# Kernel optimization log

Measured on AMD Instinct MI355X. Metric: run time of the kernel, lower is better.

Reference implementation:

```python
import jax, jax.numpy as jnp
import numpy as np

B = 2048
NUM_ITER = 3  # dynamic routing iterations


def _conv2d(x, w, b, pad):
    # x: [B,C,H,W], w: [O,I,kh,kw] (OIHW)
    y = jax.lax.conv_general_dilated(
        x, w, window_strides=(1, 1), padding=[(pad, pad), (pad, pad)],
        dimension_numbers=('NCHW', 'OIHW', 'NCHW'))
    return y + b[None, :, None, None]


def _maxpool2(x):
    return jax.lax.reduce_window(x, -jnp.inf, jax.lax.max,
                                 (1, 1, 2, 2), (1, 1, 2, 2), 'VALID')


def _squash(t, axis=-1):
    # scale = |t|^2/(1+|t|^2); out = scale * t / |t|
    n2 = jnp.sum(t * t, axis=axis, keepdims=True)
    return (n2 / (1.0 + n2)) * t * jax.lax.rsqrt(n2)


def setup_inputs() -> dict:
    key = jax.random.key(0)
    ks = jax.random.split(key, 8)
    f32 = jnp.float32
    rn = lambda k, s, sc=1.0: jax.random.normal(k, s, f32) * sc
    return {
        'x': rn(ks[0], (B, 1, 36, 60)),
        'y': rn(ks[1], (B, 2)),
        'conv1_w': rn(ks[2], (20, 1, 5, 5), 0.1),
        'conv1_b': jnp.zeros((20,), f32),
        'conv2_w': rn(ks[3], (50, 20, 5, 5), 0.01),
        'conv2_b': jnp.zeros((50,), f32),
        'pcaps_w': rn(ks[4], (16, 50, 5, 5), 0.05),   # 4 capsules x 4 out-ch, stacked
        'pcaps_b': jnp.zeros((16,), f32),
        'route_w': rn(ks[5], (2, 288, 4, 1)),          # [num_caps, route_nodes, in_ch, out_ch]
        'fc1_w': rn(ks[6], (500, 3602), 0.02),
        'fc1_b': jnp.zeros((500,), f32),
        'fc2_w': rn(ks[7], (2, 502), 0.05),
        'fc2_b': jnp.zeros((2,), f32),
    }


def reference(x, y, conv1_w, conv1_b, conv2_w, conv2_b, pcaps_w, pcaps_b,
              route_w, fc1_w, fc1_b, fc2_w, fc2_b):
    b = x.shape[0]
    # conv backbone
    h = _maxpool2(_conv2d(x, conv1_w, conv1_b, 0))   # [B,20,16,28]
    h = _maxpool2(_conv2d(h, conv2_w, conv2_b, 0))   # [B,50,6,12]

    # primary capsules: 4 parallel convs (stacked into one), each [B,4,6,12]
    p = _conv2d(h, pcaps_w, pcaps_b, 2)              # [B,16,6,12]
    u = p.reshape(b, 4, 4 * 6 * 12)                  # [B, caps=4, nodes=288] (c,h,w flatten per capsule)
    u = u.transpose(0, 2, 1)                         # [B,288,4]
    u = _squash(u, axis=-1)

    # digit capsules: dynamic routing
    # priors[k,b,r,o] = sum_c u[b,r,c] * W[k,r,c,o]
    priors = jnp.einsum('brc,krco->kbro', u, route_w)  # [2,B,288,1]
    logits = jnp.zeros_like(priors)
    v = None
    for i in range(NUM_ITER):
        probs = jax.nn.softmax(logits, axis=2)
        v = _squash(jnp.sum(probs * priors, axis=2, keepdims=True), axis=-1)  # [2,B,1,1]
        if i < NUM_ITER - 1:
            logits = logits + jnp.sum(priors * v, axis=-1, keepdims=True)

    c = v[:, :, 0, :].transpose(1, 0, 2).reshape(b, -1)  # [B,2]
    xf = h.reshape(b, -1)                                # [B,3600]
    f = jnp.concatenate([xf, c], axis=-1)                # [B,3602]
    f = jax.nn.relu(f @ fc1_w.T + fc1_b)                 # [B,500]
    f = jnp.concatenate([f, y], axis=1)                  # [B,502]
    return f @ fc2_w.T + fc2_b                           # [B,2]
```

## Files before the change

kernel.cpp:

```cpp
#include <hip/hip_runtime.h>
#include <math.h>


#define BATCH 2048
#define KP 3712
#define NPREP 551

typedef __attribute__((ext_vector_type(8))) short short8;
typedef __attribute__((ext_vector_type(4))) float floatx4;
typedef unsigned short u16;
typedef unsigned int   u32;

#define GLD(gp, lp) __builtin_amdgcn_global_load_lds( \
    (const __attribute__((address_space(1))) u32*)(gp), \
    (__attribute__((address_space(3))) u32*)(lp), 16, 0, 0)

__device__ inline float wave_sum(float v) {
#pragma unroll
    for (int off = 32; off >= 1; off >>= 1) v += __shfl_xor(v, off);
    return v;
}
__device__ inline float wave_max(float v) {
#pragma unroll
    for (int off = 32; off >= 1; off >>= 1) v = fmaxf(v, __shfl_xor(v, off));
    return v;
}
__device__ inline u16 f2bf(float f) {
    u32 u = __float_as_uint(f);
    u32 r = (u + 0x7FFFu + ((u >> 16) & 1u)) >> 16;
    return (u16)r;
}

__global__ __launch_bounds__(256, 4) void k_conv1(
    const float* __restrict__ x, const float* __restrict__ w1,
    const float* __restrict__ b1, u32* __restrict__ h1g,
    const float* __restrict__ fw,  u16* __restrict__ w_bf,
    const float* __restrict__ w2,  u16* __restrict__ w2t,
    const float* __restrict__ pcw, u16* __restrict__ w_pc,
    const float* __restrict__ f1b, const float* __restrict__ f2w,
    float* __restrict__ wtab)
{
    __shared__ __align__(16) u16 smem[20224];
    const int t  = threadIdx.x;
    const int bx = blockIdx.x;

    if (bx >= BATCH) {
        const int blk = bx - BATCH;
        if (blk < 512) {
            float* srow = (float*)smem;
            const int n = blk;
            if (n < 500) {
                const float* src = fw + (size_t)n * 3602;
                for (int i = t; i < 1800; i += 256)
                    *(float2*)&srow[2 * i] = *(const float2*)&src[2 * i];
            }
            __syncthreads();
            u32* dst = (u32*)(w_bf + (size_t)n * KP);
            for (int i = t; i < 1856; i += 256) {
                int k2 = 2 * i;
                u32 pk = 0u;
                if (n < 500 && k2 < 3600) {
                    int pos = k2 / 50, oc = k2 - 50 * pos;
                    pk = (u32)f2bf(srow[oc * 72 + pos])
                       | ((u32)f2bf(srow[(oc + 1) * 72 + pos]) << 16);
                }
                dst[i] = pk;
            }
        } else if (blk < 537) {
            int g   = (blk - 512) * 256 + t;
            int idx = g * 8;
            int tap = idx >> 11;
            int oc  = (idx >> 5) & 63;
            int ic0 = idx & 31;
            u16 v[8];
#pragma unroll
            for (int j = 0; j < 8; ++j) {
                int ic = ic0 + j;
                float f = (ic < 20 && oc < 50) ? w2[oc * 500 + ic * 25 + tap] : 0.f;
                v[j] = f2bf(f);
            }
            *(short8*)&w2t[idx] = *(short8*)v;
        } else if (blk < 550) {
            int g = (blk - 537) * 256 + t;
            if (g >= 3200) return;
            int idx = g * 8;
            int tap = idx >> 10;
            int rem = idx & 1023;
            int oc  = rem >> 6;
            int ic0 = rem & 63;
            u16 v[8];
#pragma unroll
            for (int j = 0; j < 8; ++j) {
                int ic = ic0 + j;
                float f = (ic < 50) ? pcw[(oc * 50 + ic) * 25 + tap] : 0.f;
                v[j] = f2bf(f);
            }
            *(short8*)&w_pc[idx] = *(short8*)v;
        } else {
            for (int nn = t; nn < 512; nn += 256) {
                float bias = 0.f, wc0 = 0.f, wc1 = 0.f, f20 = 0.f, f21 = 0.f;
                if (nn < 500) {
                    bias = f1b[nn];
                    wc0  = fw[(size_t)nn * 3602 + 3600];
                    wc1  = fw[(size_t)nn * 3602 + 3601];
                    f20  = f2w[nn];
                    f21  = f2w[502 + nn];
                }
                *(float4*)&wtab[nn * 8]     = make_float4(bias, wc0, wc1, f20);
                *(float4*)&wtab[nn * 8 + 4] = make_float4(f21, 0.f, 0.f, 0.f);
            }
        }
        return;
    }

    u16* xbf = smem;
    u16* im2 = smem + 2304;
    u16* h1s = smem + 11264;
    const int b = bx;

    const float* xb = x + b * 2160;
    for (int i = t; i < 2160; i += 256) {
        int r = i / 60, c = i - 60 * r;
        xbf[r * 64 + c] = f2bf(xb[i]);
    }
    __syncthreads();

    const int lane = t & 63, w = t >> 6;
    const int r16  = lane & 15;
    const int q    = lane >> 4;

    short8 w1f[2];
#pragma unroll
    for (int nt = 0; nt < 2; ++nt) {
        int n = nt * 16 + r16;
        union { short8 s; u16 a[8]; } wf;
#pragma unroll
        for (int j = 0; j < 8; ++j) {
            int k = q * 8 + j;
            float f = (n < 20 && k < 25) ? w1[n * 25 + k] : 0.f;
            wf.a[j] = f2bf(f);
        }
        w1f[nt] = wf.s;
    }

    const bool bact = (t < 224);
    const int lc_  = t / 112;
    const int pl_  = t - 112 * lc_;
    const int px_  = pl_ >> 2;
    const int dy_  = (pl_ & 3) >> 1, dx_ = pl_ & 1;
    const int xc_  = 2 * px_ + dx_;
    const int j0_  = xc_ >> 1;
    const int par_ = xc_ & 1;
    const int sw_  = (t >> 3) & 3;

#pragma unroll 1
    for (int g = 0; g < 8; ++g) {
        if (bact) {
            int c = 2 * g + lc_;
            u16 tap[25];
#pragma unroll
            for (int r = 0; r < 5; ++r) {
                const u32* U = (const u32*)&xbf[(2 * c + dy_ + r) * 64];
                u32 A0 = U[j0_], A1 = U[j0_ + 1], A2 = U[j0_ + 2];
                u16 e0 = par_ ? (u16)(A0 >> 16) : (u16)A0;
                u16 e1 = par_ ? (u16)A1         : (u16)(A0 >> 16);
                u16 e2 = par_ ? (u16)(A1 >> 16) : (u16)A1;
                u16 e3 = par_ ? (u16)A2         : (u16)(A1 >> 16);
                u16 e4 = par_ ? (u16)(A2 >> 16) : (u16)A2;
                tap[r * 5 + 0] = e0; tap[r * 5 + 1] = e1; tap[r * 5 + 2] = e2;
                tap[r * 5 + 3] = e3; tap[r * 5 + 4] = e4;
            }
            u32 ow[16];
#pragma unroll
            for (int j = 0; j < 12; ++j)
                ow[j] = (u32)tap[2 * j] | ((u32)tap[2 * j + 1] << 16);
            ow[12] = (u32)tap[24];
            ow[13] = 0u; ow[14] = 0u; ow[15] = 0u;
            u32* dst = (u32*)&im2[t * 40];
            *(uint4*)&dst[(0 ^ sw_) * 4] = make_uint4(ow[0],  ow[1],  ow[2],  ow[3]);
            *(uint4*)&dst[(1 ^ sw_) * 4] = make_uint4(ow[4],  ow[5],  ow[6],  ow[7]);
            *(uint4*)&dst[(2 ^ sw_) * 4] = make_uint4(ow[8],  ow[9],  ow[10], ow[11]);
            *(uint4*)&dst[(3 ^ sw_) * 4] = make_uint4(ow[12], ow[13], ow[14], ow[15]);
        }
        __syncthreads();
#pragma unroll
        for (int mi = 0; mi < 4; ++mi) {
            int mt = w + 4 * mi;
            if (mt < 14) {
                int m  = mt * 16 + r16;
                int sr = (m >> 3) & 3;
                short8 af = *(const short8*)&im2[m * 40 + ((q ^ sr) * 8)];
                floatx4 a1[2] = {};
#pragma unroll
                for (int nt = 0; nt < 2; ++nt)
                    a1[nt] = __builtin_amdgcn_mfma_f32_16x16x32_bf16(
                        af, w1f[nt], a1[nt], 0, 0, 0);
                int ci  = mt / 7;
                int mtl = mt - 7 * ci;
                int c   = 2 * g + ci;
                int pq  = mtl * 4 + q;
#pragma unroll
                for (int nt = 0; nt < 2; ++nt) {
                    int oc = nt * 16 + r16;
                    if (oc < 20) {
                        floatx4 a = a1[nt];
                        float v = fmaxf(fmaxf(a[0], a[1]), fmaxf(a[2], a[3]))
                                + b1[oc];
                        h1s[(c * 28 + pq) * 20 + oc] = f2bf(v);
                    }
                }
            }
        }
        __syncthreads();
    }

    u32* hg = h1g + (size_t)b * 4480;
    for (int i = t; i < 4480; i += 256) hg[i] = ((u32*)h1s)[i];
}

__global__ __launch_bounds__(256, 4) void k_conv2p(
    const u32* __restrict__ h1g, const u16* __restrict__ w2t,
    const float* __restrict__ b2, const u16* __restrict__ w_pc,
    const float* __restrict__ pcb, const float* __restrict__ rw,
    u32* __restrict__ h_bf, float* __restrict__ cbuf)
{
    __shared__ __align__(16) u16 smem[12688];
    u16* h1t = smem;

    const int t = threadIdx.x;
    const int b = blockIdx.x;

    {
        const u32* hg = h1g + (size_t)b * 4480;
#pragma unroll 1
        for (int r0 = t; r0 < 448; r0 += 256) {
            const u32* src = hg + r0 * 10;
            u32* dstp = (u32*)h1t + r0 * 12;
            uint2 a0 = *(const uint2*)(src);
            uint2 a1 = *(const uint2*)(src + 2);
            uint2 a2 = *(const uint2*)(src + 4);
            uint2 a3 = *(const uint2*)(src + 6);
            uint2 a4 = *(const uint2*)(src + 8);
            *(uint4*)(dstp)      = make_uint4(a0.x, a0.y, a1.x, a1.y);
            *(uint4*)(dstp + 4)  = make_uint4(a2.x, a2.y, a3.x, a3.y);
            *(uint4*)(dstp + 8)  = make_uint4(a4.x, a4.y, 0u, 0u);
        }
        if (t < 8) ((u32*)h1t)[5376 + t] = 0u;
    }
    __syncthreads();

    const int lane = t & 63, w = t >> 6;
    const int r16  = lane & 15;
    const int q    = lane >> 4;

    int abase[5];
#pragma unroll
    for (int i = 0; i < 5; ++i) {
        int mt = w + 4 * i;
        if (mt < 18) {
            int m  = mt * 16 + r16;
            int pq = m >> 2, sub = m & 3;
            int py = pq / 12, px = pq - py * 12;
            int yy = py * 2 + (sub >> 1);
            int xx = px * 2 + (sub & 1);
            abase[i] = (yy * 28 + xx) * 24 + q * 8;
        } else abase[i] = 0;
    }
    floatx4 acc2[5][4] = {};
    const u16* wtb = w2t + r16 * 32 + q * 8;

    short8 bf[4];
#pragma unroll
    for (int nt = 0; nt < 4; ++nt)
        bf[nt] = *(const short8*)&wtb[nt * 512];

#pragma unroll 1
    for (int tap = 0; tap < 25; ++tap) {
        short8 bfn[4];
        if (tap < 24) {
#pragma unroll
            for (int nt = 0; nt < 4; ++nt)
                bfn[nt] = *(const short8*)&wtb[(tap + 1) * 2048 + nt * 512];
        }
        int r = tap / 5, s = tap - 5 * r;
        int aoff = r * 672 + s * 24;
#pragma unroll
        for (int i = 0; i < 5; ++i) {
            int mt = w + 4 * i;
            if (mt < 18) {
                short8 af = *(const short8*)&h1t[abase[i] + aoff];
#pragma unroll
                for (int nt = 0; nt < 4; ++nt)
                    acc2[i][nt] = __builtin_amdgcn_mfma_f32_16x16x32_bf16(
                        af, bf[nt], acc2[i][nt], 0, 0, 0);
            }
        }
#pragma unroll
        for (int nt = 0; nt < 4; ++nt) bf[nt] = bfn[nt];
    }
    __syncthreads();

    for (int i = t; i < 6336; i += 256) ((u32*)smem)[i] = 0u;
    __syncthreads();

    u16* hsbuf = smem;
#pragma unroll
    for (int i = 0; i < 5; ++i) {
        int mt = w + 4 * i;
        if (mt < 18) {
            int pq = mt * 4 + q;
            int ph = pq / 12, pw = pq - 12 * ph;
#pragma unroll
            for (int nt = 0; nt < 4; ++nt) {
                int oc = nt * 16 + r16;
                if (oc < 50) {
                    floatx4 a = acc2[i][nt];
                    float v = fmaxf(fmaxf(a[0], a[1]), fmaxf(a[2], a[3])) + b2[oc];
                    hsbuf[((ph + 2) * 16 + pw + 2) * 72 + oc] = f2bf(v);
                }
            }
        }
    }
    __syncthreads();

    u32* ho = h_bf + (size_t)b * 1856;
    for (int i = t; i < 1856; i += 256) {
        u32 pk = 0u;
        if (i < 1800) {
            int k2 = 2 * i;
            int pos = k2 / 50;
            int oc  = k2 - 50 * pos;
            int ph  = pos / 12, pw = pos - 12 * ph;
            pk = ((const u32*)hsbuf)[((((ph + 2) * 16) + pw + 2) * 72 + oc) >> 1];
        }
        ho[i] = pk;
    }

    int pbase[5];
#pragma unroll
    for (int mt = 0; mt < 5; ++mt) {
        int m  = mt * 16 + r16;
        int ph = m / 12, pw = m - 12 * ph;
        pbase[mt] = (ph * 16 + pw) * 72 + q * 8;
    }
    floatx4 pacc[5] = {};
    const u16* wp = w_pc + r16 * 64 + q * 8;
    const int ntap = (28 - w) >> 2;
#pragma unroll 1
    for (int tt = 0; tt < ntap; ++tt) {
        int tap = w + 4 * tt;
        short8 b0 = *(const short8*)&wp[tap * 1024];
        short8 b1 = *(const short8*)&wp[tap * 1024 + 32];
        int r = tap / 5, s = tap - 5 * r;
        int aoff = (r * 16 + s) * 72;
#pragma unroll
        for (int mt = 0; mt < 5; ++mt) {
            short8 a0 = *(const short8*)&hsbuf[pbase[mt] + aoff];
            short8 a1 = *(const short8*)&hsbuf[pbase[mt] + aoff + 32];
            pacc[mt] = __builtin_amdgcn_mfma_f32_16x16x32_bf16(a0, b0, pacc[mt], 0, 0, 0);
            pacc[mt] = __builtin_amdgcn_mfma_f32_16x16x32_bf16(a1, b1, pacc[mt], 0, 0, 0);
        }
    }
    __syncthreads();

    float* psum = (float*)smem;
#pragma unroll
    for (int mt = 0; mt < 5; ++mt)
#pragma unroll
        for (int i = 0; i < 4; ++i) {
            int m = mt * 16 + q * 4 + i;
            psum[w * 1360 + m * 17 + r16] = pacc[mt][i];
        }
    __syncthreads();

    for (int i = t; i < 1152; i += 256) {
        int m = i >> 4, oc = i & 15;
        int a = m * 17 + oc;
        float s = psum[a] + psum[1360 + a] + psum[2720 + a] + psum[4080 + a]
                + pcb[oc];
        psum[a] = s;
    }
    __syncthreads();

    float* pri = (float*)(smem + 10880);
    for (int r = t; r < 288; r += 256) {
        int sub = r / 72;
        int pos = r - sub * 72;
        float u0 = psum[pos * 17 + 0  + sub];
        float u1 = psum[pos * 17 + 4  + sub];
        float u2 = psum[pos * 17 + 8  + sub];
        float u3 = psum[pos * 17 + 12 + sub];
        float n2 = u0 * u0 + u1 * u1 + u2 * u2 + u3 * u3;
        float scale = (n2 / (1.0f + n2)) * rsqrtf(n2);
        u0 *= scale; u1 *= scale; u2 *= scale; u3 *= scale;
#pragma unroll
        for (int k = 0; k < 2; ++k) {
            const float4 wv = *(const float4*)&rw[(k * 288 + r) * 4];
            pri[k * 288 + r] = u0 * wv.x + u1 * wv.y + u2 * wv.z + u3 * wv.w;
        }
    }
    __syncthreads();

    if (w < 2) {
        const float* pr = &pri[w * 288];
        float p[5];
        bool  val[5];
#pragma unroll
        for (int j = 0; j < 5; ++j) {
            int r  = j * 64 + lane;
            val[j] = r < 288;
            p[j]   = val[j] ? pr[r] : 0.0f;
        }
        float tot = wave_sum(p[0] + p[1] + p[2] + p[3] + p[4]);
        float s = tot * (1.0f / 288.0f);
        float a = s * fabsf(s) / (1.0f + s * s);
#pragma unroll
        for (int it = 0; it < 2; ++it) {
            float l[5];
            float lm = -INFINITY;
#pragma unroll
            for (int j = 0; j < 5; ++j) {
                l[j] = val[j] ? p[j] * a : -INFINITY;
                lm   = fmaxf(lm, l[j]);
            }
            lm = wave_max(lm);
            float se = 0.f, sp = 0.f;
#pragma unroll
            for (int j = 0; j < 5; ++j) {
                float e = val[j] ? expf(l[j] - lm) : 0.f;
                se += e;
                sp += e * p[j];
            }
            se = wave_sum(se);
            sp = wave_sum(sp);
            float sv = sp / se;
            float v  = sv * fabsf(sv) / (1.0f + sv * sv);
            if (it == 0) a += v;
            else if (lane == 0) cbuf[b * 2 + w] = v;
        }
    }
}

__global__ __launch_bounds__(256) void k_fc1(
    const u16* __restrict__ h_bf, const u16* __restrict__ w_bf,
    float* __restrict__ f1buf)
{
    __shared__ __align__(16) u16 As[64 * 32];
    __shared__ __align__(16) u16 Bs[64 * 32];
    const int t = threadIdx.x;
    const int lane = t & 63, w = t >> 6;
    const int m0 = blockIdx.x * 64;
    const int n0 = blockIdx.y * 64;
    const int s  = blockIdx.z;
    const int k0 = s * 928;

    const u16* ga = h_bf + (size_t)(m0 + (t >> 2)) * KP + k0 + (t & 3) * 8;
    const u16* gb = w_bf + (size_t)(n0 + (t >> 2)) * KP + k0 + (t & 3) * 8;
    u16* lA = As + w * 512;
    u16* lB = Bs + w * 512;

    const int r16 = lane & 15, q = lane >> 4;
    const int ar = (w * 16 + r16) * 32 + q * 8;
    const int br = r16 * 32 + q * 8;

    floatx4 acc[4] = {};
#pragma unroll 1
    for (int it = 0; it < 29; ++it) {
        const int ko = it * 32;
        GLD(ga + ko, lA);
        GLD(gb + ko, lB);
        __syncthreads();
        short8 af = *(const short8*)&As[ar];
#pragma unroll
        for (int nt = 0; nt < 4; ++nt) {
            short8 bfv = *(const short8*)&Bs[br + nt * 512];
            acc[nt] = __builtin_amdgcn_mfma_f32_16x16x32_bf16(af, bfv, acc[nt], 0, 0, 0);
        }
        __syncthreads();
    }

    float* fo = f1buf + (size_t)s * (2048 * 512);
    const int mb = m0 + w * 16;
#pragma unroll
    for (int nt = 0; nt < 4; ++nt) {
        int n = n0 + nt * 16 + r16;
#pragma unroll
        for (int i = 0; i < 4; ++i) {
            int m = mb + q * 4 + i;
            fo[(size_t)m * 512 + n] = acc[nt][i];
        }
    }
}

__global__ __launch_bounds__(256) void k_fc2(
    const float* __restrict__ f1buf, const float* __restrict__ wtab,
    const float* __restrict__ cc, const float* __restrict__ y,
    const float* __restrict__ f2w, const float* __restrict__ f2b,
    float* __restrict__ out)
{
    const int b = blockIdx.x * 4 + (threadIdx.x >> 6);
    const int lane = threadIdx.x & 63;
    const float* fb = f1buf + (size_t)b * 512;
    const float c0 = cc[b * 2], c1 = cc[b * 2 + 1];
    float s0 = 0.f, s1 = 0.f;
#pragma unroll
    for (int j = 0; j < 8; ++j) {
        int n = lane + j * 64;
        float raw = fb[n] + fb[1048576 + n] + fb[2097152 + n] + fb[3145728 + n];
        float4 t0 = *(const float4*)&wtab[n * 8];
        float  f21 = wtab[n * 8 + 4];
        float v = fmaxf(raw + t0.x + c0 * t0.y + c1 * t0.z, 0.f);
        s0 += v * t0.w;
        s1 += v * f21;
    }
    s0 = wave_sum(s0);
    s1 = wave_sum(s1);
    if (lane == 0) {
        float y0 = y[b * 2], y1 = y[b * 2 + 1];
        out[b * 2]     = s0 + f2b[0] + y0 * f2w[500] + y1 * f2w[501];
        out[b * 2 + 1] = s1 + f2b[1] + y0 * f2w[1002] + y1 * f2w[1003];
    }
}

extern "C" void kernel_launch(void* const* d_in, const int* in_sizes, int n_in,
                              void* d_out, int out_size, void* d_ws, size_t ws_size,
                              hipStream_t stream) {
    const float* x    = (const float*)d_in[0];
    const float* y    = (const float*)d_in[1];
    const float* c1w  = (const float*)d_in[2];
    const float* c1b  = (const float*)d_in[3];
    const float* c2w  = (const float*)d_in[4];
    const float* c2b  = (const float*)d_in[5];
    const float* pcw  = (const float*)d_in[6];
    const float* pcb  = (const float*)d_in[7];
    const float* rw   = (const float*)d_in[8];
    const float* f1w  = (const float*)d_in[9];
    const float* f1b  = (const float*)d_in[10];
    const float* f2w  = (const float*)d_in[11];
    const float* f2b  = (const float*)d_in[12];
    float* out = (float*)d_out;

    u32*   h_bf  = (u32*)d_ws;
    u16*   w_bf  = (u16*)(h_bf + (size_t)BATCH * 1856);
    u16*   w2t   = w_bf + (size_t)512 * KP;
    u16*   w_pc  = w2t + 51200;
    float* cbuf  = (float*)(w_pc + 25600);
    float* wtab  = cbuf + 4096;
    float* f1buf = wtab + 4096;
    u32*   h1g   = (u32*)f1buf;

    k_conv1<<<BATCH + NPREP, 256, 0, stream>>>(
        x, c1w, c1b, h1g, f1w, w_bf, c2w, w2t, pcw, w_pc, f1b, f2w, wtab);
    k_conv2p<<<BATCH, 256, 0, stream>>>(h1g, w2t, c2b, w_pc, pcb, rw,
                                        h_bf, cbuf);
    dim3 g4(32, 8, 4);
    k_fc1<<<g4, 256, 0, stream>>>((const u16*)h_bf, w_bf, f1buf);
    k_fc2<<<BATCH / 4, 256, 0, stream>>>(f1buf, wtab, cbuf, y, f2w, f2b, out);
}
```

Before: 230.5 us.

## Fuse conv1 and conv2/primary-caps kernels, keep h1 in LDS

Merges the conv1 kernel and the conv2+primary-capsule kernel into one per-sample kernel, so the conv1 output stays in shared memory in the padded layout conv2 expects instead of being written to and reread from global memory. The conv2 and primary-capsule weight conversions move into a small separate prep kernel launched first, so the fused kernel can consume them. The cost is larger LDS per block and a lower occupancy hint (3 blocks instead of 4), plus one extra tiny launch.

New measurement: 230.9 us. Within noise of the previous version (+0.2%).

```diff
diff --git a/kernel.cpp b/kernel.cpp
--- a/kernel.cpp
+++ b/kernel.cpp
@@ -4,7 +4,7 @@
 
 #define BATCH 2048
 #define KP 3712
-#define NPREP 551
+#define NPREP 513
 
 typedef __attribute__((ext_vector_type(8))) short short8;
 typedef __attribute__((ext_vector_type(4))) float floatx4;
@@ -31,16 +31,55 @@
     return (u16)r;
 }
 
-__global__ __launch_bounds__(256, 4) void k_conv1(
+__global__ __launch_bounds__(256) void k_prep0(
+    const float* __restrict__ w2,  u16* __restrict__ w2t,
+    const float* __restrict__ pcw, u16* __restrict__ w_pc)
+{
+    const int blk = blockIdx.x, t = threadIdx.x;
+    if (blk < 25) {
+        int g   = blk * 256 + t;
+        int idx = g * 8;
+        int tap = idx >> 11;
+        int oc  = (idx >> 5) & 63;
+        int ic0 = idx & 31;
+        u16 v[8];
+#pragma unroll
+        for (int j = 0; j < 8; ++j) {
+            int ic = ic0 + j;
+            float f = (ic < 20 && oc < 50) ? w2[oc * 500 + ic * 25 + tap] : 0.f;
+            v[j] = f2bf(f);
+        }
+        *(short8*)&w2t[idx] = *(short8*)v;
+    } else {
+        int g = (blk - 25) * 256 + t;
+        if (g >= 3200) return;
+        int idx = g * 8;
+        int tap = idx >> 10;
+        int rem = idx & 1023;
+        int oc  = rem >> 6;
+        int ic0 = rem & 63;
+        u16 v[8];
+#pragma unroll
+        for (int j = 0; j < 8; ++j) {
+            int ic = ic0 + j;
+            float f = (ic < 50) ? pcw[(oc * 50 + ic) * 25 + tap] : 0.f;
+            v[j] = f2bf(f);
+        }
+        *(short8*)&w_pc[idx] = *(short8*)v;
+    }
+}
+
+__global__ __launch_bounds__(256, 3) void k_convs(
     const float* __restrict__ x, const float* __restrict__ w1,
-    const float* __restrict__ b1, u32* __restrict__ h1g,
+    const float* __restrict__ b1, const u16* __restrict__ w2t,
+    const float* __restrict__ b2, const u16* __restrict__ w_pc,
+    const float* __restrict__ pcb, const float* __restrict__ rw,
+    u32* __restrict__ h_bf, float* __restrict__ cbuf,
     const float* __restrict__ fw,  u16* __restrict__ w_bf,
-    const float* __restrict__ w2,  u16* __restrict__ w2t,
-    const float* __restrict__ pcw, u16* __restrict__ w_pc,
     const float* __restrict__ f1b, const float* __restrict__ f2w,
     float* __restrict__ wtab)
 {
-    __shared__ __align__(16) u16 smem[20224];
+    __shared__ __align__(16) u16 smem[22032];
     const int t  = threadIdx.x;
     const int bx = blockIdx.x;
 
@@ -66,36 +105,6 @@
                 }
                 dst[i] = pk;
             }
-        } else if (blk < 537) {
-            int g   = (blk - 512) * 256 + t;
-            int idx = g * 8;
-            int tap = idx >> 11;
-            int oc  = (idx >> 5) & 63;
-            int ic0 = idx & 31;
-            u16 v[8];
-#pragma unroll
-            for (int j = 0; j < 8; ++j) {
-                int ic = ic0 + j;
-                float f = (ic < 20 && oc < 50) ? w2[oc * 500 + ic * 25 + tap] : 0.f;
-                v[j] = f2bf(f);
-            }
-            *(short8*)&w2t[idx] = *(short8*)v;
-        } else if (blk < 550) {
-            int g = (blk - 537) * 256 + t;
-            if (g >= 3200) return;
-            int idx = g * 8;
-            int tap = idx >> 10;
-            int rem = idx & 1023;
-            int oc  = rem >> 6;
-            int ic0 = rem & 63;
-            u16 v[8];
-#pragma unroll
-            for (int j = 0; j < 8; ++j) {
-                int ic = ic0 + j;
-                float f = (ic < 50) ? pcw[(oc * 50 + ic) * 25 + tap] : 0.f;
-                v[j] = f2bf(f);
-            }
-            *(short8*)&w_pc[idx] = *(short8*)v;
         } else {
             for (int nn = t; nn < 512; nn += 256) {
                 float bias = 0.f, wc0 = 0.f, wc1 = 0.f, f20 = 0.f, f21 = 0.f;
@@ -115,7 +124,7 @@
 
     u16* xbf = smem;
     u16* im2 = smem + 2304;
-    u16* h1s = smem + 11264;
+    u16* h1t = smem + 11264;
     const int b = bx;
 
     const float* xb = x + b * 2160;
@@ -123,6 +132,11 @@
         int r = i / 60, c = i - 60 * r;
         xbf[r * 64 + c] = f2bf(xb[i]);
     }
+    for (int i = t; i < 896; i += 256) {
+        int row = i >> 1, c = i & 1;
+        ((u32*)h1t)[row * 12 + 10 + c] = 0u;
+    }
+    if (t < 8) ((u32*)h1t)[5376 + t] = 0u;
     __syncthreads();
 
     const int lane = t & 63, w = t >> 6;
@@ -206,52 +220,13 @@
                         floatx4 a = a1[nt];
                         float v = fmaxf(fmaxf(a[0], a[1]), fmaxf(a[2], a[3]))
                                 + b1[oc];
-                        h1s[(c * 28 + pq) * 20 + oc] = f2bf(v);
+                        h1t[(c * 28 + pq) * 24 + oc] = f2bf(v);
                     }
                 }
             }
         }
         __syncthreads();
     }
-
-    u32* hg = h1g + (size_t)b * 4480;
-    for (int i = t; i < 4480; i += 256) hg[i] = ((u32*)h1s)[i];
-}
-
-__global__ __launch_bounds__(256, 4) void k_conv2p(
-    const u32* __restrict__ h1g, const u16* __restrict__ w2t,
-    const float* __restrict__ b2, const u16* __restrict__ w_pc,
-    const float* __restrict__ pcb, const float* __restrict__ rw,
-    u32* __restrict__ h_bf, float* __restrict__ cbuf)
-{
-    __shared__ __align__(16) u16 smem[12688];
-    u16* h1t = smem;
-
-    const int t = threadIdx.x;
-    const int b = blockIdx.x;
-
-    {
-        const u32* hg = h1g + (size_t)b * 4480;
-#pragma unroll 1
-        for (int r0 = t; r0 < 448; r0 += 256) {
-            const u32* src = hg + r0 * 10;
-            u32* dstp = (u32*)h1t + r0 * 12;
-            uint2 a0 = *(const uint2*)(src);
-            uint2 a1 = *(const uint2*)(src + 2);
-            uint2 a2 = *(const uint2*)(src + 4);
-            uint2 a3 = *(const uint2*)(src + 6);
-            uint2 a4 = *(const uint2*)(src + 8);
-            *(uint4*)(dstp)      = make_uint4(a0.x, a0.y, a1.x, a1.y);
-            *(uint4*)(dstp + 4)  = make_uint4(a2.x, a2.y, a3.x, a3.y);
-            *(uint4*)(dstp + 8)  = make_uint4(a4.x, a4.y, 0u, 0u);
-        }
-        if (t < 8) ((u32*)h1t)[5376 + t] = 0u;
-    }
-    __syncthreads();
-
-    const int lane = t & 63, w = t >> 6;
-    const int r16  = lane & 15;
-    const int q    = lane >> 4;
 
     int abase[5];
 #pragma unroll
@@ -547,12 +522,11 @@
     float* cbuf  = (float*)(w_pc + 25600);
     float* wtab  = cbuf + 4096;
     float* f1buf = wtab + 4096;
-    u32*   h1g   = (u32*)f1buf;
-
-    k_conv1<<<BATCH + NPREP, 256, 0, stream>>>(
-        x, c1w, c1b, h1g, f1w, w_bf, c2w, w2t, pcw, w_pc, f1b, f2w, wtab);
-    k_conv2p<<<BATCH, 256, 0, stream>>>(h1g, w2t, c2b, w_pc, pcb, rw,
-                                        h_bf, cbuf);
+
+    k_prep0<<<38, 256, 0, stream>>>(c2w, w2t, pcw, w_pc);
+    k_convs<<<BATCH + NPREP, 256, 0, stream>>>(
+        x, c1w, c1b, w2t, c2b, w_pc, pcb, rw, h_bf, cbuf,
+        f1w, w_bf, f1b, f2w, wtab);
     dim3 g4(32, 8, 4);
     k_fc1<<<g4, 256, 0, stream>>>((const u16*)h_bf, w_bf, f1buf);
     k_fc2<<<BATCH / 4, 256, 0, stream>>>(f1buf, wtab, cbuf, y, f2w, f2b, out);
```
